# Kernel optimization log

Hardware: AMD Instinct MI355X
Metric: run time of the kernel (lower is better)

## Reference

```python
import jax, jax.numpy as jnp
import numpy as np

H = 16        # num_attention_heads
E = 1024      # hidden_size
D = E // H    # attention_head_size = 64
M = 1024      # max_position_embeddings
EPS = 1e-12


def setup_inputs() -> dict:
    key = jax.random.key(0)
    ks = jax.random.split(key, 12)
    s = 0.02
    B, S = 8, 1024
    return {
        "hidden_states": jax.random.normal(ks[0], (B, S, E), jnp.float32),
        "Wq": jax.random.normal(ks[1], (E, E), jnp.float32) * s,
        "bq": jnp.zeros((E,), jnp.float32),
        "Wk": jax.random.normal(ks[2], (E, E), jnp.float32) * s,
        "bk": jnp.zeros((E,), jnp.float32),
        "Wv": jax.random.normal(ks[3], (E, E), jnp.float32) * s,
        "bv": jnp.zeros((E,), jnp.float32),
        "dist_emb": jax.random.normal(ks[4], (2 * M - 1, D), jnp.float32) * s,
        "Wo": jax.random.normal(ks[5], (E, E), jnp.float32) * s,
        "bo": jnp.zeros((E,), jnp.float32),
        "ln_gamma": jnp.ones((E,), jnp.float32),
        "ln_beta": jnp.zeros((E,), jnp.float32),
    }


def reference(hidden_states, Wq, bq, Wk, bk, Wv, bv, dist_emb, Wo, bo, ln_gamma, ln_beta):
    B, S, _ = hidden_states.shape

    def heads(x):  # [B,S,E] -> [B,H,S,D]
        return x.reshape(B, S, H, D).transpose(0, 2, 1, 3)

    q = heads(hidden_states @ Wq + bq)
    k = heads(hidden_states @ Wk + bk)
    v = heads(hidden_states @ Wv + bv)

    scores = jnp.einsum("bhqd,bhkd->bhqk", q, k)

    # relative_key_query positional bias
    pos_l = jnp.arange(S)[:, None]
    pos_r = jnp.arange(S)[None, :]
    dist_idx = pos_l - pos_r + M - 1            # [S,S] in [0, 2M-2]
    pos_emb = dist_emb[dist_idx]                # [S,S,D]  (l, r, d)
    rel_q = jnp.einsum("bhld,lrd->bhlr", q, pos_emb)
    rel_k = jnp.einsum("bhrd,lrd->bhlr", k, pos_emb)
    scores = (scores + rel_q + rel_k) / jnp.sqrt(jnp.asarray(D, scores.dtype))

    probs = jax.nn.softmax(scores, axis=-1)     # dropout prob = 0 (eval)
    ctx = jnp.einsum("bhqk,bhkd->bhqd", probs, v)
    ctx = ctx.transpose(0, 2, 1, 3).reshape(B, S, E)

    # BertSelfOutput: dense + residual + LayerNorm
    h = ctx @ Wo + bo + hidden_states
    mu = jnp.mean(h, axis=-1, keepdims=True)
    var = jnp.mean(jnp.square(h - mu), axis=-1, keepdims=True)
    out = (h - mu) * jax.lax.rsqrt(var + EPS) * ln_gamma + ln_beta
    return out
```

## Files before the change

kernel.cpp:

```cpp
#include <hip/hip_runtime.h>


typedef unsigned short u16;
typedef unsigned int u32;
typedef unsigned long long u64;
typedef __bf16 bf16x8 __attribute__((ext_vector_type(8)));
typedef float  f32x4  __attribute__((ext_vector_type(4)));
typedef int    i32x4  __attribute__((ext_vector_type(4)));

__device__ __forceinline__ float b2f(u16 u) {
  union { u32 i; float f; } x;
  x.i = ((u32)u) << 16;
  return x.f;
}
__device__ __forceinline__ u16 f2b_manual(float f) {
  union { float f; u32 u; } x;
  x.f = f;
  return (u16)((x.u + 0x7FFFu + ((x.u >> 16) & 1u)) >> 16);
}
#if __has_builtin(__builtin_amdgcn_cvt_pk_bf16_f32)
typedef __bf16 bf16x2 __attribute__((ext_vector_type(2)));
__device__ __forceinline__ u32 cvt2(float a, float b) {
  union { bf16x2 v; u32 u; } x;
  x.v = __builtin_amdgcn_cvt_pk_bf16_f32(a, b);
  return x.u;
}
#else
__device__ __forceinline__ u32 cvt2(float a, float b) {
  return (u32)f2b_manual(a) | ((u32)f2b_manual(b) << 16);
}
#endif
__device__ __forceinline__ u16 f2b(float f) { return (u16)(cvt2(f, f) & 0xffffu); }

union LdU { i32x4 i4; bf16x8 b8; };
__device__ __forceinline__ bf16x8 ldb8(const u16* p) {
  LdU u; u.i4 = *(const i32x4*)p; return u.b8;
}
__device__ __forceinline__ void pack8(u16* dst, const float* src) {
  f32x4 lo = *(const f32x4*)src, hi = *(const f32x4*)(src + 4);
  i32x4 v;
  v.x = (int)cvt2(lo.x, lo.y); v.y = (int)cvt2(lo.z, lo.w);
  v.z = (int)cvt2(hi.x, hi.y); v.w = (int)cvt2(hi.z, hi.w);
  *(i32x4*)dst = v;
}
#define MFMA16(a, b, c) __builtin_amdgcn_mfma_f32_16x16x32_bf16((a), (b), (c), 0, 0, 0)

template <int C>
__device__ __forceinline__ float dppmov(float x) {
  union { float f; int i; } a, r;
  a.f = x;
  r.i = __builtin_amdgcn_update_dpp(0, a.i, C, 0xF, 0xF, true);
  return r.f;
}
__device__ __forceinline__ float rsum16(float x) {
  x += dppmov<0xB1>(x);
  x += dppmov<0x4E>(x);
  x += dppmov<0x141>(x);
  x += dppmov<0x140>(x);
  return x;
}
__device__ __forceinline__ float fexp2(float x) {
#if __has_builtin(__builtin_amdgcn_exp2f)
  return __builtin_amdgcn_exp2f(x);
#else
  return exp2f(x);
#endif
}

#if __has_builtin(__builtin_amdgcn_global_load_lds)
#define HAS_GLDS 1
typedef __attribute__((address_space(3))) u32 as3_u32;
typedef const __attribute__((address_space(1))) u32 as1_u32;
__device__ __forceinline__ void gld16(const u16* g, u16* lds_wave_base) {
  __builtin_amdgcn_global_load_lds(
      (as1_u32*)g, (as3_u32*)(u32)(u64)lds_wave_base, 16, 0, 0);
}
#else
#define HAS_GLDS 0
__device__ __forceinline__ void gld16_fb(const u16* g, u16* lds_wave_base,
                                         int lane) {
  *(i32x4*)(lds_wave_base + lane * 8) = *(const i32x4*)g;
}
#endif

__global__ __launch_bounds__(256) void convX(
    const float* __restrict__ X, u16* __restrict__ Xb) {
  int i = (blockIdx.x * 256 + threadIdx.x) * 8;
  pack8(&Xb[i], &X[i]);
}

__global__ __launch_bounds__(256) void convD(
    const float* __restrict__ dist, u16* __restrict__ distb) {
  int i = (blockIdx.x * 256 + threadIdx.x) * 8;
  if (i < 2047 * 64) pack8(&distb[i], &dist[i]);
}

__global__ __launch_bounds__(256) void convWt(
    const float* __restrict__ W, u16* __restrict__ Wt) {
  __shared__ float tile[64][65];
  const int tid = threadIdx.x;
  const int k0 = blockIdx.x * 64, m0 = blockIdx.y * 64;
#pragma unroll
  for (int it = 0; it < 4; it++) {
    int row = (tid >> 4) + 16 * it;
    int col = (tid & 15) * 4;
    f32x4 v = *(const f32x4*)&W[(size_t)(k0 + row) * 1024 + m0 + col];
    tile[row][col] = v.x; tile[row][col + 1] = v.y;
    tile[row][col + 2] = v.z; tile[row][col + 3] = v.w;
  }
  __syncthreads();
#pragma unroll
  for (int it = 0; it < 4; it++) {
    int mr = (tid >> 4) + 16 * it;
    int kc = (tid & 15) * 4;
    u32 w0 = cvt2(tile[kc][mr], tile[kc + 1][mr]);
    u32 w1 = cvt2(tile[kc + 2][mr], tile[kc + 3][mr]);
    *(u64*)&Wt[(size_t)(m0 + mr) * 1024 + k0 + kc] = (u64)w0 | ((u64)w1 << 32);
  }
}

__global__ __launch_bounds__(256) void transV(
    const u16* __restrict__ V, u16* __restrict__ Vt) {
  __shared__ u16 tile[64][72];
  const int tid = threadIdx.x;
  const int bh = blockIdx.y, b = bh >> 4, h = bh & 15;
  const int s0 = blockIdx.x << 6;
  const u16* Vb = V + (size_t)(b * 1024) * 1024 + h * 64;
  {
    int rp = tid >> 3, a = tid & 7;
    const u16* src = &Vb[(size_t)(s0 + 2 * rp) * 1024 + a * 8];
    i32x4 va = *(const i32x4*)src;
    i32x4 vb2 = *(const i32x4*)(src + 1024);
    u16 ta[8] __attribute__((aligned(16)));
    u16 tb[8] __attribute__((aligned(16)));
    *(i32x4*)ta = va; *(i32x4*)tb = vb2;
    int colb = ((((rp >> 2) ^ a) << 3) | ((2 * rp) & 7));
#pragma unroll
    for (int j = 0; j < 8; j++)
      *(u32*)&tile[a * 8 + j][colb] = (u32)ta[j] | ((u32)tb[j] << 16);
  }
  __syncthreads();
  int d = tid >> 2, cc = tid & 3;
  int sw = (d >> 3) & 7;
  i32x4 lo = *(const i32x4*)&tile[d][((2 * cc) ^ sw) << 3];
  i32x4 hi = *(const i32x4*)&tile[d][((2 * cc + 1) ^ sw) << 3];
  u16* dst = Vt + ((size_t)bh * 64 + d) * 1024 + s0 + cc * 16;
  *(i32x4*)dst = lo;
  *(i32x4*)(dst + 8) = hi;
}

template <int RESID, int OUTF32>
__global__ __launch_bounds__(256) void gemm_bb(
    const u16* __restrict__ A, const u16* __restrict__ Wt,
    const float* __restrict__ bias, const float* __restrict__ resid,
    float* __restrict__ outF, u16* __restrict__ outB, int N, int K, int M) {
  __shared__ u16 sA[128 * 64];
  __shared__ u16 sW[128 * 64];

  const int tid = threadIdx.x;
  const int lane = tid & 63, w = tid >> 6;
  const int quad = lane >> 4, lb = lane & 15;
  const int m0 = blockIdx.x * 128, n0 = blockIdx.y * 128;

  const int srow = lane >> 3;
  const int gcol = ((lane & 7) ^ srow) << 3;

  f32x4 acc[2][8] = {};

  for (int k0 = 0; k0 < K; k0 += 64) {
#pragma unroll
    for (int j = 0; j < 4; j++) {
      int rb = (4 * w + j) * 8;
      const u16* ga = &A[(size_t)(n0 + rb + srow) * K + k0 + gcol];
      const u16* gw = &Wt[(size_t)(m0 + rb + srow) * K + k0 + gcol];
#if HAS_GLDS
      gld16(ga, &sA[rb * 64]);
      gld16(gw, &sW[rb * 64]);
#else
      gld16_fb(ga, &sA[rb * 64], lane);
      gld16_fb(gw, &sW[rb * 64], lane);
#endif
    }
    __syncthreads();

    const int r0 = 32 * w + lb;
    const int sw0 = r0 & 7;
    bf16x8 a00 = ldb8(&sA[r0 * 64 + ((quad ^ sw0) << 3)]);
    bf16x8 a01 = ldb8(&sA[r0 * 64 + (((4 + quad) ^ sw0) << 3)]);
    bf16x8 a10 = ldb8(&sA[(r0 + 16) * 64 + ((quad ^ sw0) << 3)]);
    bf16x8 a11 = ldb8(&sA[(r0 + 16) * 64 + (((4 + quad) ^ sw0) << 3)]);
#pragma unroll
    for (int t = 0; t < 8; t++) {
      int n = 16 * t + lb;
      int swn = n & 7;
      bf16x8 b0 = ldb8(&sW[n * 64 + ((quad ^ swn) << 3)]);
      bf16x8 b1 = ldb8(&sW[n * 64 + (((4 + quad) ^ swn) << 3)]);
      acc[0][t] = MFMA16(a00, b0, acc[0][t]);
      acc[0][t] = MFMA16(a01, b1, acc[0][t]);
      acc[1][t] = MFMA16(a10, b0, acc[1][t]);
      acc[1][t] = MFMA16(a11, b1, acc[1][t]);
    }
    __syncthreads();
  }

#pragma unroll
  for (int half = 0; half < 2; half++)
#pragma unroll
    for (int t = 0; t < 8; t++) {
      int col = m0 + 16 * t + lb;
      float bv = bias[col];
#pragma unroll
      for (int i = 0; i < 4; i++) {
        int rowg = n0 + 32 * w + 16 * half + quad * 4 + i;
        float v = acc[half][t][i] + bv;
        if (RESID) v += resid[(size_t)rowg * M + col];
        if (OUTF32) outF[(size_t)rowg * M + col] = v;
        else        outB[(size_t)rowg * M + col] = f2b(v);
      }
    }
}

__global__ __launch_bounds__(256) void attn(
    const u16* __restrict__ Q, const u16* __restrict__ Kv,
    const u16* __restrict__ Vt, const u16* __restrict__ distb,
    u16* __restrict__ ctx) {
  __shared__ u16 sQ[64][72];
  __shared__ u16 sK[64][72];
  __shared__ u16 sVt[64][72];
  __shared__ u16 sP[128][72];
  __shared__ u16 sGq[128 * 64];
  __shared__ u16 sGk[128 * 64];

  const int tid = threadIdx.x;
  const int lane = tid & 63, w = tid >> 6;
  const int quad = lane >> 4, lb = lane & 15;
  const int bh = blockIdx.y, b = bh >> 4, h = bh & 15;
  const int q0 = blockIdx.x << 6;
  const int S = 1024, E = 1024;
  const u16* Qb = Q  + (size_t)(b * S) * E + h * 64;
  const u16* Kb = Kv + (size_t)(b * S) * E + h * 64;
  const u16* Vtb = Vt + (size_t)bh * 64 * 1024;

  const int sr = tid >> 3, sc8 = (tid & 7) << 3;

  {
    *(i32x4*)&sQ[sr][sc8] = *(const i32x4*)&Qb[(size_t)(q0 + sr) * E + sc8];
    *(i32x4*)&sQ[sr + 32][sc8] =
        *(const i32x4*)&Qb[(size_t)(q0 + sr + 32) * E + sc8];
    *(i32x4*)&sK[sr][sc8] = *(const i32x4*)&Kb[(size_t)sr * E + sc8];
    *(i32x4*)&sK[sr + 32][sc8] =
        *(const i32x4*)&Kb[(size_t)(sr + 32) * E + sc8];
    *(i32x4*)&sVt[sr][sc8] = *(const i32x4*)&Vtb[(size_t)sr * 1024 + sc8];
    *(i32x4*)&sVt[sr + 32][sc8] =
        *(const i32x4*)&Vtb[(size_t)(sr + 32) * 1024 + sc8];
    const int dbase = q0 + 960;
#pragma unroll
    for (int j = 0; j < 4; j++) {
      int p = sr + 32 * j;
      int g = dbase + p;
      if (g > 2046) g = 2046;
      *(i32x4*)&sP[p][sc8] = *(const i32x4*)&distb[(size_t)g * 64 + sc8];
    }
  }
  __syncthreads();

  const int row = 16 * w + lb;
  bf16x8 aq0 = ldb8(&sQ[row][quad * 8]);
  bf16x8 aq1 = ldb8(&sQ[row][32 + quad * 8]);

  f32x4 accO[4] = {};
  float l_i[4] = {0.f, 0.f, 0.f, 0.f};
  const float C2 = 0.125f * 1.44269504f;

  for (int kt = 0; kt < 16; kt++) {
    const int xorv = (kt & 1) << 6;

    i32x4 kr0, kr1, vr0, vr1, pr0, pr1;
    if (kt < 15) {
      const int r0n = (kt + 1) << 6;
      kr0 = *(const i32x4*)&Kb[(size_t)(r0n + sr) * E + sc8];
      kr1 = *(const i32x4*)&Kb[(size_t)(r0n + sr + 32) * E + sc8];
      vr0 = *(const i32x4*)&Vtb[(size_t)sr * 1024 + r0n + sc8];
      vr1 = *(const i32x4*)&Vtb[(size_t)(sr + 32) * 1024 + r0n + sc8];
      const int dbn = q0 - r0n + 960;
      pr0 = *(const i32x4*)&distb[(size_t)(dbn + sr) * 64 + sc8];
      pr1 = *(const i32x4*)&distb[(size_t)(dbn + sr + 32) * 64 + sc8];
    }

    __builtin_amdgcn_s_setprio(1);
    f32x4 accS[4] = {};
#pragma unroll
    for (int t = 0; t < 4; t++) {
      int n = 16 * t + lb;
      bf16x8 b0 = ldb8(&sK[n][quad * 8]);
      bf16x8 b1 = ldb8(&sK[n][32 + quad * 8]);
      accS[t] = MFMA16(aq0, b0, accS[t]);
      accS[t] = MFMA16(aq1, b1, accS[t]);
    }
    bf16x8 ak0 = ldb8(&sK[row][quad * 8]);
    bf16x8 ak1 = ldb8(&sK[row][32 + quad * 8]);
#pragma unroll
    for (int u = 0; u < 8; u++) {
      int prow = (16 * u + lb) ^ xorv;
      bf16x8 p0 = ldb8(&sP[prow][quad * 8]);
      bf16x8 p1 = ldb8(&sP[prow][32 + quad * 8]);
      f32x4 gq = {}, gk = {};
      gq = MFMA16(aq0, p0, gq); gq = MFMA16(aq1, p1, gq);
      gk = MFMA16(ak0, p0, gk); gk = MFMA16(ak1, p1, gk);
      int grow = 16 * u + lb;
      int cswz = (16 * w + 4 * quad) ^ ((grow & 7) << 3);
      u16* gqb = &sGq[grow * 64 + cswz];
      u16* gkb = &sGk[grow * 64 + cswz];
      *(u32*)gqb = cvt2(gq[0], gq[1]);
      *(u32*)(gqb + 2) = cvt2(gq[2], gq[3]);
      *(u32*)gkb = cvt2(gk[0], gk[1]);
      *(u32*)(gkb + 2) = cvt2(gk[2], gk[3]);
    }
    __builtin_amdgcn_s_setprio(0);
    __syncthreads();

    float pr[4][4], rsum[4] = {0.f, 0.f, 0.f, 0.f};
#pragma unroll
    for (int t = 0; t < 4; t++) {
#pragma unroll
      for (int i = 0; i < 4; i++) {
        int rl = 16 * w + quad * 4 + i;
        int cl = 16 * t + lb;
        int c = rl - cl + 63;
        int sw8 = (c & 7) << 3;
        float s = accS[t][i] + b2f(sGq[(c << 6) | (rl ^ sw8)]) +
                  b2f(sGk[(c << 6) | (cl ^ sw8)]);
        float e = fexp2(s * C2);
        pr[t][i] = e;
        rsum[i] += e;
      }
    }
#pragma unroll
    for (int i = 0; i < 4; i++) l_i[i] += rsum16(rsum[i]);

#pragma unroll
    for (int t = 0; t < 4; t++)
#pragma unroll
      for (int i = 0; i < 4; i++)
        sK[16 * w + quad * 4 + i][16 * t + lb] = f2b(pr[t][i]);

    bf16x8 ap0 = ldb8(&sK[row][quad * 8]);
    bf16x8 ap1 = ldb8(&sK[row][32 + quad * 8]);
    __builtin_amdgcn_s_setprio(1);
#pragma unroll
    for (int t = 0; t < 4; t++) {
      int n = 16 * t + lb;
      bf16x8 v0 = ldb8(&sVt[n][quad * 8]);
      bf16x8 v1 = ldb8(&sVt[n][32 + quad * 8]);
      accO[t] = MFMA16(ap0, v0, accO[t]);
      accO[t] = MFMA16(ap1, v1, accO[t]);
    }
    __builtin_amdgcn_s_setprio(0);
    __syncthreads();

    if (kt < 15) {
      const int xn = ((kt + 1) & 1) << 6;
      *(i32x4*)&sK[sr][sc8] = kr0;
      *(i32x4*)&sK[sr + 32][sc8] = kr1;
      *(i32x4*)&sVt[sr][sc8] = vr0;
      *(i32x4*)&sVt[sr + 32][sc8] = vr1;
      *(i32x4*)&sP[sr ^ xn][sc8] = pr0;
      *(i32x4*)&sP[(sr + 32) ^ xn][sc8] = pr1;
      __syncthreads();
    }
  }

  u16* Cb = ctx + (size_t)(b * S) * E + h * 64;
#pragma unroll
  for (int t = 0; t < 4; t++)
#pragma unroll
    for (int i = 0; i < 4; i++) {
      int rl = 16 * w + quad * 4 + i;
      Cb[(size_t)(q0 + rl) * E + 16 * t + lb] = f2b(accO[t][i] / l_i[i]);
    }
}

__global__ __launch_bounds__(256) void lnorm(
    const float* __restrict__ Hp, const float* __restrict__ gamma,
    const float* __restrict__ beta, float* __restrict__ out) {
  __shared__ float red[8];
  const int rowb = blockIdx.x, tid = threadIdx.x;
  const float* hr = Hp + (size_t)rowb * 1024;
  f32x4 v = *(const f32x4*)&hr[tid * 4];
  float s = v.x + v.y + v.z + v.w;
  float q = v.x * v.x + v.y * v.y + v.z * v.z + v.w * v.w;
#pragma unroll
  for (int d = 1; d < 64; d <<= 1) {
    s += __shfl_xor(s, d, 64);
    q += __shfl_xor(q, d, 64);
  }
  int w = tid >> 6, lane = tid & 63;
  if (lane == 0) { red[w] = s; red[4 + w] = q; }
  __syncthreads();
  s = red[0] + red[1] + red[2] + red[3];
  q = red[4] + red[5] + red[6] + red[7];
  float mu = s * (1.f / 1024.f);
  float var = q * (1.f / 1024.f) - mu * mu;
  float rstd = rsqrtf(var + 1e-12f);
  float* orow = out + (size_t)rowb * 1024;
  f32x4 o;
#pragma unroll
  for (int j = 0; j < 4; j++) {
    int c = tid * 4 + j;
    o[j] = (v[j] - mu) * rstd * gamma[c] + beta[c];
  }
  *(f32x4*)&orow[tid * 4] = o;
}

extern "C" void kernel_launch(void* const* d_in, const int* in_sizes, int n_in,
                              void* d_out, int out_size, void* d_ws,
                              size_t ws_size, hipStream_t stream) {
  const float* X    = (const float*)d_in[0];
  const float* Wq   = (const float*)d_in[1];
  const float* bq   = (const float*)d_in[2];
  const float* Wk   = (const float*)d_in[3];
  const float* bk   = (const float*)d_in[4];
  const float* Wv   = (const float*)d_in[5];
  const float* bv   = (const float*)d_in[6];
  const float* dist = (const float*)d_in[7];
  const float* Wo   = (const float*)d_in[8];
  const float* bo   = (const float*)d_in[9];
  const float* gam  = (const float*)d_in[10];
  const float* bet  = (const float*)d_in[11];

  const size_t NE = (size_t)8192 * 1024;
  char* ws = (char*)d_ws;
  u16* Qw = (u16*)(ws);
  u16* Kw = (u16*)(ws + 2 * NE);
  u16* Vw = (u16*)(ws + 4 * NE);
  u16* Cw = (u16*)(ws + 6 * NE);
  float* Hp = (float*)ws;

  char* ob = (char*)d_out;
  u16* Wtq = (u16*)(ob);
  u16* Wtk = (u16*)(ob + (2u << 20));
  u16* Wtv = (u16*)(ob + (4u << 20));
  u16* Wto = (u16*)(ob + (6u << 20));
  u16* Xb  = (u16*)(ob + (8u << 20));
  u16* Vtg = (u16*)(ob + (8u << 20));
  u16* distb = (u16*)(ob + (26u << 20));

  dim3 bb(256);
  dim3 gw(16, 16);
  convWt<<<gw, bb, 0, stream>>>(Wq, Wtq);
  convWt<<<gw, bb, 0, stream>>>(Wk, Wtk);
  convWt<<<gw, bb, 0, stream>>>(Wv, Wtv);
  convWt<<<gw, bb, 0, stream>>>(Wo, Wto);
  convX<<<dim3(4096), bb, 0, stream>>>(X, Xb);
  convD<<<dim3(64), bb, 0, stream>>>(dist, distb);

  dim3 gg(8, 64);
  gemm_bb<0, 0><<<gg, bb, 0, stream>>>(Xb, Wtq, bq, nullptr, nullptr, Qw, 8192, 1024, 1024);
  gemm_bb<0, 0><<<gg, bb, 0, stream>>>(Xb, Wtk, bk, nullptr, nullptr, Kw, 8192, 1024, 1024);
  gemm_bb<0, 0><<<gg, bb, 0, stream>>>(Xb, Wtv, bv, nullptr, nullptr, Vw, 8192, 1024, 1024);
  transV<<<dim3(16, 128), bb, 0, stream>>>(Vw, Vtg);
  attn<<<dim3(16, 128), bb, 0, stream>>>(Qw, Kw, Vtg, distb, Cw);
  gemm_bb<1, 1><<<gg, bb, 0, stream>>>(Cw, Wto, bo, X, Hp, nullptr, 8192, 1024, 1024);
  lnorm<<<dim3(8192), bb, 0, stream>>>(Hp, gam, bet, (float*)d_out);
}
```

Before: 446.2 us.

## Skip unused relative-position MFMA tiles and fold softmax scale into Q/K

In the attention kernel each wave now computes only the positional-bias tiles (q·dist and k·dist) that its own rows actually read, instead of all eight 16-row tiles, which cuts MFMA and LDS work in the bias stage. The softmax scale times log2(e) is split as a square-root factor folded into the Q and K GEMM epilogues and into the dist-embedding conversion, removing a multiply per score. Shared-memory and global addresses are precomputed as pointers and advanced per tile, and the row-sum cross-lane reduction moves out of the loop to run once at the end. The pre-scaling changes bf16 rounding slightly, and the per-wave branching adds divergence-free but irregular control flow.

```diff
diff --git a/kernel.cpp b/kernel.cpp
--- a/kernel.cpp
+++ b/kernel.cpp
@@ -83,6 +83,8 @@
 }
 #endif
 
+#define SQRT_C2 0.42466090f
+
 __global__ __launch_bounds__(256) void convX(
     const float* __restrict__ X, u16* __restrict__ Xb) {
   int i = (blockIdx.x * 256 + threadIdx.x) * 8;
@@ -92,7 +94,12 @@
 __global__ __launch_bounds__(256) void convD(
     const float* __restrict__ dist, u16* __restrict__ distb) {
   int i = (blockIdx.x * 256 + threadIdx.x) * 8;
-  if (i < 2047 * 64) pack8(&distb[i], &dist[i]);
+  if (i < 2047 * 64) {
+    float t[8];
+#pragma unroll
+    for (int j = 0; j < 8; j++) t[j] = dist[i + j] * SQRT_C2;
+    pack8(&distb[i], t);
+  }
 }
 
 __global__ __launch_bounds__(256) void convWt(
@@ -153,7 +160,8 @@
 __global__ __launch_bounds__(256) void gemm_bb(
     const u16* __restrict__ A, const u16* __restrict__ Wt,
     const float* __restrict__ bias, const float* __restrict__ resid,
-    float* __restrict__ outF, u16* __restrict__ outB, int N, int K, int M) {
+    float* __restrict__ outF, u16* __restrict__ outB, int N, int K, int M,
+    float oscale) {
   __shared__ u16 sA[128 * 64];
   __shared__ u16 sW[128 * 64];
 
@@ -214,6 +222,7 @@
         int rowg = n0 + 32 * w + 16 * half + quad * 4 + i;
         float v = acc[half][t][i] + bv;
         if (RESID) v += resid[(size_t)rowg * M + col];
+        v *= oscale;
         if (OUTF32) outF[(size_t)rowg * M + col] = v;
         else        outB[(size_t)rowg * M + col] = f2b(v);
       }
@@ -268,90 +277,123 @@
   bf16x8 aq0 = ldb8(&sQ[row][quad * 8]);
   bf16x8 aq1 = ldb8(&sQ[row][32 + quad * 8]);
 
+  const u16* kb  = &sK[lb][quad * 8];
+  const u16* vbp = &sVt[lb][quad * 8];
+  const u16* akb = &sK[row][quad * 8];
+  const u16* pb  = &sP[lb][quad * 8];
+  u16* gqsb = &sGq[lb * 64 + ((16 * w + 4 * quad) ^ ((lb & 7) << 3))];
+  u16* gksb = &sGk[lb * 64 + ((16 * w + 4 * quad) ^ ((lb & 7) << 3))];
+  u16* psb  = &sK[16 * w + 4 * quad][lb];
+  const int rl_ = 16 * w + 4 * quad;
+  const u16* gqa_[4];
+  const u16* gka_[4][4];
+#pragma unroll
+  for (int i = 0; i < 4; i++) {
+    int rl = rl_ + i;
+    int c3 = rl - lb + 15;
+    int sw8 = (c3 & 7) << 3;
+    gqa_[i] = &sGq[(c3 << 6) + (rl ^ sw8)];
+#pragma unroll
+    for (int t = 0; t < 4; t++) {
+      int c = rl - (16 * t + lb) + 63;
+      gka_[i][t] = &sGk[(c << 6) + ((16 * t + lb) ^ sw8)];
+    }
+  }
+  const u16* kg0 = Kb + (size_t)(64 + sr) * E + sc8;
+  const u16* kg1 = kg0 + (size_t)32 * E;
+  const u16* vg0 = Vtb + (size_t)sr * 1024 + 64 + sc8;
+  const u16* vg1 = vg0 + (size_t)32 * 1024;
+  const u16* dg0 = distb + (size_t)(q0 - 64 + 960 + sr) * 64 + sc8;
+  const u16* dg1 = dg0 + (size_t)32 * 64;
+  u16* wk0 = &sK[sr][sc8];  u16* wk1 = &sK[sr + 32][sc8];
+  u16* wv0 = &sVt[sr][sc8]; u16* wv1 = &sVt[sr + 32][sc8];
+  u16* wp0 = &sP[sr][sc8];  u16* wp1 = &sP[sr + 32][sc8];
+
+  const int uqlo = w, uqhi = w + 4;
+  const int uklo = 3 - w, ukhi = 7 - w;
+
   f32x4 accO[4] = {};
   float l_i[4] = {0.f, 0.f, 0.f, 0.f};
-  const float C2 = 0.125f * 1.44269504f;
 
   for (int kt = 0; kt < 16; kt++) {
     const int xorv = (kt & 1) << 6;
 
-    i32x4 kr0, kr1, vr0, vr1, pr0, pr1;
+    i32x4 kr0, kr1, vr0, vr1, dr0, dr1;
     if (kt < 15) {
-      const int r0n = (kt + 1) << 6;
-      kr0 = *(const i32x4*)&Kb[(size_t)(r0n + sr) * E + sc8];
-      kr1 = *(const i32x4*)&Kb[(size_t)(r0n + sr + 32) * E + sc8];
-      vr0 = *(const i32x4*)&Vtb[(size_t)sr * 1024 + r0n + sc8];
-      vr1 = *(const i32x4*)&Vtb[(size_t)(sr + 32) * 1024 + r0n + sc8];
-      const int dbn = q0 - r0n + 960;
-      pr0 = *(const i32x4*)&distb[(size_t)(dbn + sr) * 64 + sc8];
-      pr1 = *(const i32x4*)&distb[(size_t)(dbn + sr + 32) * 64 + sc8];
+      kr0 = *(const i32x4*)kg0;
+      kr1 = *(const i32x4*)kg1;
+      vr0 = *(const i32x4*)vg0;
+      vr1 = *(const i32x4*)vg1;
+      dr0 = *(const i32x4*)dg0;
+      dr1 = *(const i32x4*)dg1;
     }
 
     __builtin_amdgcn_s_setprio(1);
     f32x4 accS[4] = {};
 #pragma unroll
     for (int t = 0; t < 4; t++) {
-      int n = 16 * t + lb;
-      bf16x8 b0 = ldb8(&sK[n][quad * 8]);
-      bf16x8 b1 = ldb8(&sK[n][32 + quad * 8]);
+      bf16x8 b0 = ldb8(kb + 1152 * t);
+      bf16x8 b1 = ldb8(kb + 1152 * t + 32);
       accS[t] = MFMA16(aq0, b0, accS[t]);
       accS[t] = MFMA16(aq1, b1, accS[t]);
     }
-    bf16x8 ak0 = ldb8(&sK[row][quad * 8]);
-    bf16x8 ak1 = ldb8(&sK[row][32 + quad * 8]);
+    bf16x8 ak0 = ldb8(akb);
+    bf16x8 ak1 = ldb8(akb + 32);
+    const u16* pbA = pb + (xorv ? 4608 : 0);
+    const u16* pbB = pb + (xorv ? -4608 : 0);
 #pragma unroll
     for (int u = 0; u < 8; u++) {
-      int prow = (16 * u + lb) ^ xorv;
-      bf16x8 p0 = ldb8(&sP[prow][quad * 8]);
-      bf16x8 p1 = ldb8(&sP[prow][32 + quad * 8]);
-      f32x4 gq = {}, gk = {};
-      gq = MFMA16(aq0, p0, gq); gq = MFMA16(aq1, p1, gq);
-      gk = MFMA16(ak0, p0, gk); gk = MFMA16(ak1, p1, gk);
-      int grow = 16 * u + lb;
-      int cswz = (16 * w + 4 * quad) ^ ((grow & 7) << 3);
-      u16* gqb = &sGq[grow * 64 + cswz];
-      u16* gkb = &sGk[grow * 64 + cswz];
-      *(u32*)gqb = cvt2(gq[0], gq[1]);
-      *(u32*)(gqb + 2) = cvt2(gq[2], gq[3]);
-      *(u32*)gkb = cvt2(gk[0], gk[1]);
-      *(u32*)(gkb + 2) = cvt2(gk[2], gk[3]);
+      const bool doq = (u >= uqlo) && (u <= uqhi);
+      const bool dok = (u >= uklo) && (u <= ukhi);
+      if (doq || dok) {
+        const u16* pp = (u < 4 ? pbA : pbB) + 1152 * u;
+        bf16x8 p0 = ldb8(pp);
+        bf16x8 p1 = ldb8(pp + 32);
+        if (doq) {
+          f32x4 gq = {};
+          gq = MFMA16(aq0, p0, gq);
+          gq = MFMA16(aq1, p1, gq);
+          *(u32*)(gqsb + 1024 * u) = cvt2(gq[0], gq[1]);
+          *(u32*)(gqsb + 1024 * u + 2) = cvt2(gq[2], gq[3]);
+        }
+        if (dok) {
+          f32x4 gk = {};
+          gk = MFMA16(ak0, p0, gk);
+          gk = MFMA16(ak1, p1, gk);
+          *(u32*)(gksb + 1024 * u) = cvt2(gk[0], gk[1]);
+          *(u32*)(gksb + 1024 * u + 2) = cvt2(gk[2], gk[3]);
+        }
+      }
     }
     __builtin_amdgcn_s_setprio(0);
     __syncthreads();
 
-    float pr[4][4], rsum[4] = {0.f, 0.f, 0.f, 0.f};
+    float pr[4][4];
 #pragma unroll
     for (int t = 0; t < 4; t++) {
 #pragma unroll
       for (int i = 0; i < 4; i++) {
-        int rl = 16 * w + quad * 4 + i;
-        int cl = 16 * t + lb;
-        int c = rl - cl + 63;
-        int sw8 = (c & 7) << 3;
-        float s = accS[t][i] + b2f(sGq[(c << 6) | (rl ^ sw8)]) +
-                  b2f(sGk[(c << 6) | (cl ^ sw8)]);
-        float e = fexp2(s * C2);
+        float s = accS[t][i] + b2f(gqa_[i][1024 * (3 - t)]) +
+                  b2f(*gka_[i][t]);
+        float e = fexp2(s);
         pr[t][i] = e;
-        rsum[i] += e;
+        l_i[i] += e;
       }
     }
-#pragma unroll
-    for (int i = 0; i < 4; i++) l_i[i] += rsum16(rsum[i]);
 
 #pragma unroll
     for (int t = 0; t < 4; t++)
 #pragma unroll
       for (int i = 0; i < 4; i++)
-        sK[16 * w + quad * 4 + i][16 * t + lb] = f2b(pr[t][i]);
-
-    bf16x8 ap0 = ldb8(&sK[row][quad * 8]);
-    bf16x8 ap1 = ldb8(&sK[row][32 + quad * 8]);
+        psb[72 * i + 16 * t] = f2b(pr[t][i]);
+
+    bf16x8 ap0 = ldb8(akb);
+    bf16x8 ap1 = ldb8(akb + 32);
     __builtin_amdgcn_s_setprio(1);
 #pragma unroll
     for (int t = 0; t < 4; t++) {
-      int n = 16 * t + lb;
-      bf16x8 v0 = ldb8(&sVt[n][quad * 8]);
-      bf16x8 v1 = ldb8(&sVt[n][32 + quad * 8]);
+      bf16x8 v0 = ldb8(vbp + 1152 * t);
+      bf16x8 v1 = ldb8(vbp + 1152 * t + 32);
       accO[t] = MFMA16(ap0, v0, accO[t]);
       accO[t] = MFMA16(ap1, v1, accO[t]);
     }
@@ -359,16 +401,22 @@
     __syncthreads();
 
     if (kt < 15) {
-      const int xn = ((kt + 1) & 1) << 6;
-      *(i32x4*)&sK[sr][sc8] = kr0;
-      *(i32x4*)&sK[sr + 32][sc8] = kr1;
-      *(i32x4*)&sVt[sr][sc8] = vr0;
-      *(i32x4*)&sVt[sr + 32][sc8] = vr1;
-      *(i32x4*)&sP[sr ^ xn][sc8] = pr0;
-      *(i32x4*)&sP[(sr + 32) ^ xn][sc8] = pr1;
+      const int pxn = ((kt + 1) & 1) ? 4608 : 0;
+      *(i32x4*)wk0 = kr0;
+      *(i32x4*)wk1 = kr1;
+      *(i32x4*)wv0 = vr0;
+      *(i32x4*)wv1 = vr1;
+      *(i32x4*)(wp0 + pxn) = dr0;
+      *(i32x4*)(wp1 + pxn) = dr1;
+      kg0 += (size_t)64 * E; kg1 += (size_t)64 * E;
+      vg0 += 64;             vg1 += 64;
+      dg0 -= 64 * 64;        dg1 -= 64 * 64;
       __syncthreads();
     }
   }
+
+#pragma unroll
+  for (int i = 0; i < 4; i++) l_i[i] = rsum16(l_i[i]);
 
   u16* Cb = ctx + (size_t)(b * S) * E + h * 64;
 #pragma unroll
@@ -455,11 +503,11 @@
   convD<<<dim3(64), bb, 0, stream>>>(dist, distb);
 
   dim3 gg(8, 64);
-  gemm_bb<0, 0><<<gg, bb, 0, stream>>>(Xb, Wtq, bq, nullptr, nullptr, Qw, 8192, 1024, 1024);
-  gemm_bb<0, 0><<<gg, bb, 0, stream>>>(Xb, Wtk, bk, nullptr, nullptr, Kw, 8192, 1024, 1024);
-  gemm_bb<0, 0><<<gg, bb, 0, stream>>>(Xb, Wtv, bv, nullptr, nullptr, Vw, 8192, 1024, 1024);
+  gemm_bb<0, 0><<<gg, bb, 0, stream>>>(Xb, Wtq, bq, nullptr, nullptr, Qw, 8192, 1024, 1024, SQRT_C2);
+  gemm_bb<0, 0><<<gg, bb, 0, stream>>>(Xb, Wtk, bk, nullptr, nullptr, Kw, 8192, 1024, 1024, SQRT_C2);
+  gemm_bb<0, 0><<<gg, bb, 0, stream>>>(Xb, Wtv, bv, nullptr, nullptr, Vw, 8192, 1024, 1024, 1.0f);
   transV<<<dim3(16, 128), bb, 0, stream>>>(Vw, Vtg);
   attn<<<dim3(16, 128), bb, 0, stream>>>(Qw, Kw, Vtg, distb, Cw);
-  gemm_bb<1, 1><<<gg, bb, 0, stream>>>(Cw, Wto, bo, X, Hp, nullptr, 8192, 1024, 1024);
+  gemm_bb<1, 1><<<gg, bb, 0, stream>>>(Cw, Wto, bo, X, Hp, nullptr, 8192, 1024, 1024, 1.0f);
   lnorm<<<dim3(8192), bb, 0, stream>>>(Hp, gam, bet, (float*)d_out);
 }
```

After: 431.2 us. 3.4% less time.
